# Performance work log

Measured on AMD Instinct MI355X. Metric: run time of the kernel, lower is better.

The kernel has to match this reference:

```python
import jax, jax.numpy as jnp
import numpy as np

B, C, H, W = 4, 256, 64, 64


def _radius_bias(h, w):
    # Attention_Radius: grid coords (x: 1..W, y: H..1), pairwise euclidean dist
    y = jnp.arange(h, 0, -1, dtype=jnp.float32)
    x = jnp.arange(1, w + 1, dtype=jnp.float32)
    yy, xx = jnp.meshgrid(y, x, indexing='ij')
    coords = jnp.stack([xx.reshape(-1), yy.reshape(-1)], axis=1)  # [N,2]
    diff = coords[:, None, :] - coords[None, :, :]                # [N,N,2]
    dist = jnp.sqrt(jnp.sum(diff * diff, axis=-1))                # [N,N]
    # Weight_Mapping: linearly map to [0.5,2] with inversion (far -> small)
    lo, hi = jnp.float32(0.5), jnp.float32(2.0)
    return hi - (dist - dist.min()) * (hi - lo) / (dist.max() - dist.min())


def setup_inputs() -> dict:
    key = jax.random.key(0)
    k1, k2, k3, k4 = jax.random.split(key, 4)
    scale = 1.0 / np.sqrt(C)
    return {
        'x': jax.random.normal(k1, (B, C, H, W), dtype=jnp.float32),
        'w_phi': jax.random.normal(k2, (C, C), dtype=jnp.float32) * scale,
        'w_theta': jax.random.normal(k3, (C, C), dtype=jnp.float32) * scale,
        'w_g': jax.random.normal(k4, (C, C), dtype=jnp.float32) * scale,
    }


def reference(x, w_phi, w_theta, w_g):
    b, c, h, w = x.shape
    n = h * w
    xf = x.reshape(b, c, n)                                  # [b,c,N]
    phi = jnp.einsum('dc,bcn->bdn', w_phi, xf)               # [b,c,N]
    theta = jnp.einsum('dc,bcn->bnd', w_theta, xf)           # [b,N,c]
    g = jnp.einsum('dc,bcn->bnd', w_g, xf)                   # [b,N,c]
    scores = jnp.einsum('bnc,bcm->bnm', theta, phi)          # [b,N,N]
    scores = _radius_bias(h, w) * scores                     # multiplicative radius bias
    attn = jax.nn.softmax(scores, axis=1)                    # NOTE: softmax over dim=1 (rows)
    out = jnp.einsum('bnm,bmc->bnc', attn, g)                # [b,N,c]
    out = out.transpose(0, 2, 1).reshape(b, c, h, w)
    return out + x
```

## Files before the change

kernel.cpp:

```cpp
#include <hip/hip_runtime.h>
#include <math.h>

typedef unsigned short ush;
typedef short short8 __attribute__((ext_vector_type(8)));
typedef int i32x4 __attribute__((ext_vector_type(4)));
typedef int i32x16 __attribute__((ext_vector_type(16)));
typedef float f32x16 __attribute__((ext_vector_type(16)));
typedef unsigned int u32;

namespace {
constexpr int B = 4, C = 256, N = 4096, NCH = 4;
constexpr size_t PL8 = (size_t)B * N * C;
constexpr size_t OFF_TH  = 0;
constexpr size_t OFF_TL  = PL8;
constexpr size_t OFF_PH  = 2 * PL8;
constexpr size_t OFF_PLO = 3 * PL8;
constexpr size_t OFF_G   = 4 * PL8;
constexpr size_t FOFF    = 4 * PL8 + (size_t)B * C * N * 2;
constexpr size_t F_PM = 0;
constexpr size_t F_PS = (size_t)B * NCH * N;
constexpr size_t F_M  = 2 * (size_t)B * NCH * N;

constexpr size_t OFF_XH = 26ull * 1024 * 1024;
constexpr size_t OFF_XL = OFF_XH + (size_t)B * N * C * 2;
constexpr size_t OFF_WH = OFF_XL + (size_t)B * N * C * 2;
constexpr size_t OFF_WL = OFF_WH + (size_t)3 * C * C * 2;
constexpr size_t WS_NEED = OFF_WL + (size_t)3 * C * C * 2;

constexpr float SCL = 8.0f / 127.0f;
constexpr float S2  = SCL * SCL;
constexpr float RB  = 1.5f / 89.09545f;
constexpr float L2E = 1.44269504f;
constexpr float BA2  = 2.0f * S2 * L2E;
constexpr float BBC2 = RB * S2 * L2E;
constexpr float C1  = 1.0f / 254.0f;
constexpr float INV_SCL = 127.0f / 8.0f;
}

#define MFMAI8(a, b, c)  __builtin_amdgcn_mfma_i32_32x32x32_i8((a), (b), (c), 0, 0, 0)
#define MFMABF(a, b, c)  __builtin_amdgcn_mfma_f32_32x32x16_bf16((a), (b), (c), 0, 0, 0)

#define WAITV(n) asm volatile("s_waitcnt vmcnt(" #n ")" ::: "memory")
#define WAITVL(n) asm volatile("s_waitcnt vmcnt(" #n ") lgkmcnt(0)" ::: "memory")
#define PBAR __builtin_amdgcn_s_barrier()

__device__ __forceinline__ float fast_exp2(float x) {
#if __has_builtin(__builtin_amdgcn_exp2f)
  return __builtin_amdgcn_exp2f(x);
#else
  float r; asm("v_exp_f32 %0, %1" : "=v"(r) : "v"(x)); return r;
#endif
}
__device__ __forceinline__ float fast_sqrt(float x) {
#if __has_builtin(__builtin_amdgcn_sqrtf)
  return __builtin_amdgcn_sqrtf(x);
#else
  float r; asm("v_sqrt_f32 %0, %1" : "=v"(r) : "v"(x)); return r;
#endif
}

__device__ __forceinline__ ush f2bf(float v) {
  u32 x = __float_as_uint(v);
  return (ush)((x + 0x7FFFu + ((x >> 16) & 1u)) >> 16);
}
__device__ __forceinline__ float bf2f(ush h) {
  return __uint_as_float(((u32)h) << 16);
}

__device__ __forceinline__ float score_i(int hh, int xx, int d2i) {
  float u = fmaf((float)xx, C1, (float)hh);
  float d = fast_sqrt((float)d2i);
  return fmaf(d, -BBC2, BA2) * u;
}

__device__ __forceinline__ void gload16(const void* g, void* l) {
  __builtin_amdgcn_global_load_lds(
      (const __attribute__((address_space(1))) u32*)(g),
      (__attribute__((address_space(3))) u32*)(l), 16, 0, 0);
}

__global__ __launch_bounds__(256) void proj_kernel(
    const float* __restrict__ x, const float* __restrict__ w_phi,
    const float* __restrict__ w_theta, const float* __restrict__ w_g,
    char* __restrict__ wsu8) {
  __shared__ float Wst[16][68];
  __shared__ float Xs[16][68];
  const int tid = threadIdx.x, tx = tid & 15, ty = tid >> 4;
  const int b = blockIdx.y / 3, p = blockIdx.y % 3;
  const int c0 = (blockIdx.x >> 6) * 64;
  const int nb = (blockIdx.x & 63) * 64;
  const float* w = (p == 0) ? w_theta : (p == 1) ? w_phi : w_g;

  float acc[4][4] = {};
  for (int kk = 0; kk < C; kk += 16) {
    {
      int r = tid >> 2, kq = (tid & 3) << 2;
      float4 v = *reinterpret_cast<const float4*>(&w[(size_t)(c0 + r) * C + kk + kq]);
      Wst[kq + 0][r] = v.x; Wst[kq + 1][r] = v.y;
      Wst[kq + 2][r] = v.z; Wst[kq + 3][r] = v.w;
    }
    {
      int k = tid >> 4, j4 = (tid & 15) << 2;
      *reinterpret_cast<float4*>(&Xs[k][j4]) =
          *reinterpret_cast<const float4*>(&x[((size_t)b * C + kk + k) * N + nb + j4]);
    }
    __syncthreads();
#pragma unroll
    for (int k2 = 0; k2 < 16; ++k2) {
      float4 av = *reinterpret_cast<const float4*>(&Wst[k2][ty << 2]);
      float4 bv = *reinterpret_cast<const float4*>(&Xs[k2][tx << 2]);
      float aa[4] = {av.x, av.y, av.z, av.w};
      float bb[4] = {bv.x, bv.y, bv.z, bv.w};
#pragma unroll
      for (int i = 0; i < 4; ++i)
#pragma unroll
        for (int j = 0; j < 4; ++j) acc[i][j] = fmaf(aa[i], bb[j], acc[i][j]);
    }
    __syncthreads();
  }

  if (p < 2) {
    char* hi = wsu8 + (p == 0 ? OFF_TH : OFF_PH) + (size_t)b * N * C;
    char* lo = wsu8 + (p == 0 ? OFF_TL : OFF_PLO) + (size_t)b * N * C;
#pragma unroll
    for (int j = 0; j < 4; ++j) {
      int n = nb + (tx << 2) + j;
      u32 ph = 0, pl = 0;
#pragma unroll
      for (int i = 0; i < 4; ++i) {
        float t = acc[i][j] * INV_SCL;
        int h = __float2int_rn(t);
        h = max(-127, min(127, h));
        int l = __float2int_rn((t - (float)h) * 254.0f);
        l = max(-127, min(127, l));
        ph |= ((u32)(h & 0xFF)) << (8 * i);
        pl |= ((u32)(l & 0xFF)) << (8 * i);
      }
      *(u32*)(hi + (size_t)n * C + c0 + (ty << 2)) = ph;
      *(u32*)(lo + (size_t)n * C + c0 + (ty << 2)) = pl;
    }
  } else {
    ush* gp = (ush*)(wsu8 + OFF_G) + (size_t)b * C * N;
#pragma unroll
    for (int i = 0; i < 4; ++i) {
      ushort4 pk;
      pk.x = f2bf(acc[i][0]); pk.y = f2bf(acc[i][1]);
      pk.z = f2bf(acc[i][2]); pk.w = f2bf(acc[i][3]);
      *reinterpret_cast<ushort4*>(&gp[(size_t)(c0 + (ty << 2) + i) * N + nb + (tx << 2)]) = pk;
    }
  }
}

__global__ __launch_bounds__(256) void split_x(
    const float* __restrict__ x, char* __restrict__ wsu8) {
  __shared__ float Ls[64 * 66];
  const int tid = threadIdx.x;
  const int n0 = blockIdx.x * 64, c0 = blockIdx.y * 64, b = blockIdx.z;
  const float* xb = x + ((size_t)b * C + c0) * N + n0;
#pragma unroll
  for (int i = 0; i < 4; ++i) {
    int fi = i * 256 + tid, cc = fi >> 4, c4 = fi & 15;
    float4 v = *reinterpret_cast<const float4*>(xb + (size_t)cc * N + c4 * 4);
    Ls[cc * 66 + c4 * 4 + 0] = v.x; Ls[cc * 66 + c4 * 4 + 1] = v.y;
    Ls[cc * 66 + c4 * 4 + 2] = v.z; Ls[cc * 66 + c4 * 4 + 3] = v.w;
  }
  __syncthreads();
  ush* XH = (ush*)(wsu8 + OFF_XH) + ((size_t)b * N + n0) * C + c0;
  ush* XL = (ush*)(wsu8 + OFF_XL) + ((size_t)b * N + n0) * C + c0;
#pragma unroll
  for (int i = 0; i < 4; ++i) {
    int oi = i * 256 + tid, n = oi >> 4, c4 = oi & 15;
    ushort4 hv, lv;
#pragma unroll
    for (int j = 0; j < 4; ++j) {
      float v = Ls[(c4 * 4 + j) * 66 + n];
      ush h = f2bf(v);
      ush l = f2bf(v - bf2f(h));
      (&hv.x)[j] = h; (&lv.x)[j] = l;
    }
    *reinterpret_cast<ushort4*>(XH + (size_t)n * C + c4 * 4) = hv;
    *reinterpret_cast<ushort4*>(XL + (size_t)n * C + c4 * 4) = lv;
  }
}

__global__ __launch_bounds__(256) void split_w(
    const float* __restrict__ w_phi, const float* __restrict__ w_theta,
    const float* __restrict__ w_g, char* __restrict__ wsu8) {
  int id = blockIdx.x * 256 + threadIdx.x;
  int p = id / 16384, e4 = id % 16384;
  const float* w = (p == 0) ? w_theta : (p == 1) ? w_phi : w_g;
  float4 v = *reinterpret_cast<const float4*>(w + (size_t)e4 * 4);
  ush* WH = (ush*)(wsu8 + OFF_WH) + (size_t)p * C * C + (size_t)e4 * 4;
  ush* WL = (ush*)(wsu8 + OFF_WL) + (size_t)p * C * C + (size_t)e4 * 4;
  ushort4 hv, lv;
  float vv[4] = {v.x, v.y, v.z, v.w};
#pragma unroll
  for (int j = 0; j < 4; ++j) {
    ush h = f2bf(vv[j]);
    ush l = f2bf(vv[j] - bf2f(h));
    (&hv.x)[j] = h; (&lv.x)[j] = l;
  }
  *reinterpret_cast<ushort4*>(WH) = hv;
  *reinterpret_cast<ushort4*>(WL) = lv;
}

__global__ __launch_bounds__(512) void proj_mfma(char* __restrict__ wsu8) {
  __shared__ __align__(16) char plds[131072];
  const int tid = threadIdx.x, lane = tid & 63, w = tid >> 6;
  const int l31 = lane & 31, lh5 = lane >> 5;
  const int wr = w >> 2, wc = w & 3;
  const int bx = blockIdx.x;
  const int db = (bx >> 5) * 64, nb = (bx & 31) * 128;
  const int b = blockIdx.y / 3, p = blockIdx.y % 3;
  const char* xh = wsu8 + OFF_XH + (size_t)b * N * C * 2;
  const char* xl = wsu8 + OFF_XL + (size_t)b * N * C * 2;
  const char* wh = wsu8 + OFF_WH + (size_t)p * C * C * 2;
  const char* wl = wsu8 + OFF_WL + (size_t)p * C * C * 2;
  char* const Wb = plds;
  char* const Xb = plds + 65536;

#pragma unroll
  for (int cix = 0; cix < 8; ++cix) {
    int pl = cix >> 2, ci = cix & 3;
    int glin = ci * 512 + tid;
    int d = glin >> 5, g = glin & 31;
    const char* src = (pl ? wl : wh) + (size_t)(db + d) * 512 + ((g ^ (d & 15)) << 4);
    gload16(src, Wb + pl * 32768 + ci * 8192 + (tid << 4));
  }
  auto stageX = [&](int ch, int buf) {
#pragma unroll
    for (int cix = 0; cix < 4; ++cix) {
      int pl = cix >> 1, ci = cix & 1;
      int glin = ci * 512 + tid;
      int n = glin >> 3, g = glin & 7;
      const char* src = (pl ? xl : xh) +
          (size_t)(nb + n) * 512 + ch * 128 + ((g ^ (n & 7)) << 4);
      gload16(src, Xb + buf * 32768 + pl * 16384 + ci * 8192 + (tid << 4));
    }
  };
  stageX(0, 0);
  __syncthreads();

  const int arow = wr * 32 + l31;
  const int brow = wc * 32 + l31;
  f32x16 acc = {};
  for (int ch = 0; ch < 4; ++ch) {
    if (ch < 3) stageX(ch + 1, (ch + 1) & 1);
    const char* XB = Xb + (ch & 1) * 32768;
    __builtin_amdgcn_s_setprio(1);
#pragma unroll
    for (int kt = 0; kt < 4; ++kt) {
      int slw = (ch * 4 + kt) * 2 + lh5;
      int oW = ((slw ^ (arow & 15)) << 4);
      short8 wa = *(const short8*)(Wb + arow * 512 + oW);
      short8 wb2 = *(const short8*)(Wb + 32768 + arow * 512 + oW);
      int slx = kt * 2 + lh5;
      int oX = ((slx ^ (brow & 7)) << 4);
      short8 xa = *(const short8*)(XB + brow * 128 + oX);
      short8 xb2 = *(const short8*)(XB + 16384 + brow * 128 + oX);
      acc = MFMABF(wa, xa, acc);
      acc = MFMABF(wa, xb2, acc);
      acc = MFMABF(wb2, xa, acc);
    }
    __builtin_amdgcn_s_setprio(0);
    __syncthreads();
  }

  const int n = nb + wc * 32 + l31;
  if (p < 2) {
    char* hi = wsu8 + (p == 0 ? OFF_TH : OFF_PH) + (size_t)b * N * C;
    char* lo = wsu8 + (p == 0 ? OFF_TL : OFF_PLO) + (size_t)b * N * C;
#pragma unroll
    for (int q = 0; q < 4; ++q) {
      u32 phv = 0, plv = 0;
#pragma unroll
      for (int j = 0; j < 4; ++j) {
        float t = acc[q * 4 + j] * INV_SCL;
        int h = __float2int_rn(t);
        h = max(-127, min(127, h));
        int l = __float2int_rn((t - (float)h) * 254.0f);
        l = max(-127, min(127, l));
        phv |= ((u32)(h & 0xFF)) << (8 * j);
        plv |= ((u32)(l & 0xFF)) << (8 * j);
      }
      int dd = db + wr * 32 + 8 * q + 4 * lh5;
      *(u32*)(hi + (size_t)n * C + dd) = phv;
      *(u32*)(lo + (size_t)n * C + dd) = plv;
    }
  } else {
    ush* gp = (ush*)(wsu8 + OFF_G) + (size_t)b * C * N;
#pragma unroll
    for (int r = 0; r < 16; ++r) {
      int dd = db + wr * 32 + (r & 3) + 8 * (r >> 2) + 4 * lh5;
      gp[(size_t)dd * N + n] = f2bf(acc[r]);
    }
  }
}

__global__ __launch_bounds__(512, 4) void stats_kernel(
    const char* __restrict__ wsu8, float* __restrict__ fws) {
  __shared__ __align__(16) char lds[65536];
  const int tid = threadIdx.x, lane = tid & 63, w = tid >> 6;
  const int l31 = lane & 31, lh5 = lane >> 5;
  const int wr = w >> 2, wc = w & 3;
  int flat = (blockIdx.z * NCH + blockIdx.y) * 32 + blockIdx.x;
  int nf = ((flat & 7) << 6) | (flat >> 3);
  const int b = nf >> 7, rem = nf & 127, chunk = rem >> 5, mt = rem & 31;
  const int mb = mt * 128, cbase = chunk * 1024;
  const size_t bo = (size_t)b * N * C;
  const char* th  = wsu8 + OFF_TH + bo;
  const char* tl  = wsu8 + OFF_TL + bo;
  const char* ph  = wsu8 + OFF_PH + bo;
  const char* plo = wsu8 + OFF_PLO + bo;

  const int brow = wc * 32 + l31;
  const int bswz = brow & 15;
  i32x4 FH[8];
  {
    const char* prh = ph + (size_t)(mb + brow) * C + lh5 * 16;
#pragma unroll
    for (int q = 0; q < 8; ++q) FH[q] = *(const i32x4*)(prh + q * 32);
  }
#pragma unroll
  for (int cix = 0; cix < 4; ++cix) {
    int rl = cix * 32 + w * 4 + (lane >> 4);
    int gc = lane & 15;
    const char* src = plo + (size_t)(mb + rl) * C + ((gc ^ (rl & 15)) << 4);
    gload16(src, lds + cix * 8192 + w * 1024 + lane * 16);
  }
  char* const T0 = lds + 32768;
  char* const T1 = lds + 49152;

  auto stage = [&](int s, char* dst) {
    int ntx = s >> 1, h = s & 1;
    int rl = w * 8 + (lane >> 3);
    int gc = lane & 7;
#pragma unroll
    for (int plane = 0; plane < 2; ++plane) {
      const char* src = (plane ? tl : th) +
          (size_t)(cbase + ntx * 64 + rl) * C + h * 128 + ((gc ^ (rl & 7)) << 4);
      gload16(src, dst + plane * 8192 + w * 1024 + lane * 16);
    }
  };
  stage(0, T0);
  __syncthreads();

  const int m = mb + brow;
  const int mcl = m & 63, mh = m >> 6;
  const int arow = wr * 32 + l31;
  const int aswz = arow & 7;
  const int nbl = wr * 32;
  float rmax = -3e38f, rsum = 0.0f;

  u32 dxp[8];
#pragma unroll
  for (int r2 = 0; r2 < 8; ++r2) {
    int r0i = 2 * r2, r1i = 2 * r2 + 1;
    int p0 = (r0i & 3) + 8 * (r0i >> 2) + 4 * lh5;
    int p1 = (r1i & 3) + 8 * (r1i >> 2) + 4 * lh5;
    int d0 = nbl + p0 - mcl, d1 = nbl + p1 - mcl;
    dxp[r2] = (u32)(d0 * d0) | ((u32)(d1 * d1) << 16);
  }

  char* Tc = T0; char* Tn = T1;
  for (int nt = 0; nt < 16; ++nt) {
    i32x16 HH = {}, XX = {};
#pragma unroll
    for (int h = 0; h < 2; ++h) {
      int p = nt * 2 + h;
      if (p < 31) stage(p + 1, Tn);
      __builtin_amdgcn_s_setprio(1);
#pragma unroll
      for (int kt = 0; kt < 4; ++kt) {
        int g = h * 4 + kt;
        int ga = (((kt * 2 + lh5) ^ aswz) << 4);
        i32x4 ah = *(const i32x4*)(Tc + arow * 128 + ga);
        i32x4 al = *(const i32x4*)(Tc + 8192 + arow * 128 + ga);
        int gb = (((g * 2 + lh5) ^ bswz) << 4);
        i32x4 bl = *(const i32x4*)(lds + brow * 256 + gb);
        HH = MFMAI8(ah, FH[g], HH);
        XX = MFMAI8(ah, bl, XX);
        XX = MFMAI8(al, FH[g], XX);
      }
      __builtin_amdgcn_s_setprio(0);
      if (h == 1) {
        int dyi = (cbase >> 6) + nt - mh;
        int dy2i = dyi * dyi;
        float bs[16];
#pragma unroll
        for (int r = 0; r < 16; ++r) {
          int d2i = (int)((dxp[r >> 1] >> ((r & 1) * 16)) & 0xFFFFu) + dy2i;
          bs[r] = score_i(HH[r], XX[r], d2i);
        }
        float m0 = fmaxf(fmaxf(fmaxf(bs[0], bs[1]), fmaxf(bs[2], bs[3])),
                         fmaxf(fmaxf(bs[4], bs[5]), fmaxf(bs[6], bs[7])));
        float m1 = fmaxf(fmaxf(fmaxf(bs[8], bs[9]), fmaxf(bs[10], bs[11])),
                         fmaxf(fmaxf(bs[12], bs[13]), fmaxf(bs[14], bs[15])));
        float nm = fmaxf(rmax, fmaxf(m0, m1));
#pragma unroll
        for (int r = 0; r < 16; ++r) bs[r] = fast_exp2(bs[r] - nm);
        float s0 = ((bs[0] + bs[1]) + (bs[2] + bs[3])) + ((bs[4] + bs[5]) + (bs[6] + bs[7]));
        float s1 = ((bs[8] + bs[9]) + (bs[10] + bs[11])) + ((bs[12] + bs[13]) + (bs[14] + bs[15]));
        rsum = fmaf(rsum, fast_exp2(rmax - nm), s0 + s1);
        rmax = nm;
      }
      __syncthreads();
      char* t = Tc; Tc = Tn; Tn = t;
    }
  }
  {
    float om = __shfl_xor(rmax, 32);
    float os = __shfl_xor(rsum, 32);
    float nm = fmaxf(rmax, om);
    rsum = rsum * fast_exp2(rmax - nm) + os * fast_exp2(om - nm);
    rmax = nm;
  }
  float* redM = (float*)lds;
  float* redS = (float*)(lds + 1024);
  if (lane < 32) {
    redM[wr * 128 + wc * 32 + l31] = rmax;
    redS[wr * 128 + wc * 32 + l31] = rsum;
  }
  __syncthreads();
  if (tid < 128) {
    float m0 = redM[tid], m1 = redM[128 + tid];
    float nm = fmaxf(m0, m1);
    float s = redS[tid] * fast_exp2(m0 - nm) + redS[128 + tid] * fast_exp2(m1 - nm);
    fws[F_PM + ((size_t)(b * NCH + chunk)) * N + mb + tid] = nm;
    fws[F_PS + ((size_t)(b * NCH + chunk)) * N + mb + tid] = s;
  }
}

__global__ __launch_bounds__(256) void finalize_stats(float* __restrict__ fws) {
  int id = blockIdx.x * 256 + threadIdx.x;
  if (id >= B * N) return;
  int b = id >> 12, m = id & (N - 1);
  float M = -3e38f;
#pragma unroll
  for (int ch = 0; ch < NCH; ++ch)
    M = fmaxf(M, fws[F_PM + (size_t)(b * NCH + ch) * N + m]);
  float S = 0.0f;
#pragma unroll
  for (int ch = 0; ch < NCH; ++ch)
    S += fws[F_PS + (size_t)(b * NCH + ch) * N + m] *
         fast_exp2(fws[F_PM + (size_t)(b * NCH + ch) * N + m] - M);
  fws[F_M + id] = M + __log2f(S);
}

__global__ __launch_bounds__(512, 1) void out_kernel(
    const float* __restrict__ x, float* __restrict__ out,
    const char* __restrict__ wsu8, const float* __restrict__ fws) {
  __shared__ __align__(16) char lds[131072];
  const int tid = threadIdx.x, lane = tid & 63, w = tid >> 6;
  const int l31 = lane & 31, lh5 = lane >> 5;
  const int wn = w >> 2, wm = w & 3;
  int flat = blockIdx.y * gridDim.x + blockIdx.x;
  int nf = ((flat & 7) << 5) | (flat >> 3);
  const int b = nf >> 6, ntile = nf & 63;
  const int n0 = ntile * 64;
  const size_t bo = (size_t)b * N * C;
  const char* th  = wsu8 + OFF_TH + bo;
  const char* tl  = wsu8 + OFF_TL + bo;
  const char* ph  = wsu8 + OFF_PH + bo;
  const char* plo = wsu8 + OFF_PLO + bo;
  const char* GPB = wsu8 + OFF_G + (size_t)b * C * N * 2;
  const float* Qv = fws + F_M + (size_t)b * N;

  char* const R0 = lds;
  char* const R1 = lds + 32768;
  char* const R2 = lds + 65536;
  char* const Pb = lds + 98304;
  char* const Qb = lds + 114688;

  const int arow = wn * 32 + l31;
  const int brow = wm * 32 + l31;
  const int grow = w * 32 + l31;
  const int bswz = brow & 7, gswz = grow & 7;
  const int mcl = (wm * 32 + l31) & 63;

  i32x4 TH[8], TL[8];
  {
    const char* trh = th + (size_t)(n0 + arow) * C + lh5 * 16;
    const char* trl = tl + (size_t)(n0 + arow) * C + lh5 * 16;
#pragma unroll
    for (int q = 0; q < 8; ++q) {
      TH[q] = *(const i32x4*)(trh + q * 32);
      TL[q] = *(const i32x4*)(trl + q * 32);
    }
  }
  u32 dxp[8];
#pragma unroll
  for (int r2 = 0; r2 < 8; ++r2) {
    int r0i = 2 * r2, r1i = 2 * r2 + 1;
    int p0i = wn * 32 + (r0i & 3) + 8 * (r0i >> 2) + 4 * lh5;
    int p1i = wn * 32 + (r1i & 3) + 8 * (r1i >> 2) + 4 * lh5;
    int d0 = p0i - mcl, d1 = p1i - mcl;
    dxp[r2] = (u32)(d0 * d0) | ((u32)(d1 * d1) << 16);
  }
#pragma unroll
  for (int i = 0; i < 2; ++i)
    gload16((const char*)Qv + i * 8192 + w * 1024 + lane * 16,
            Qb + i * 8192 + w * 1024 + lane * 16);

  auto stagePhi = [&](int mrow0, int khalf, char* dst) {
#pragma unroll
    for (int cix = 0; cix < 4; ++cix) {
      int plane = cix >> 1, q = cix & 1;
      int rl = q * 64 + w * 8 + (lane >> 3);
      int gc = lane & 7;
      const char* src = (plane ? plo : ph) +
          (size_t)(mrow0 + rl) * C + khalf * 128 + ((gc ^ (rl & 7)) << 4);
      gload16(src, dst + plane * 16384 + q * 8192 + w * 1024 + lane * 16);
    }
  };
  auto stageG = [&](int m0g, char* dst) {
#pragma unroll
    for (int cix = 0; cix < 4; ++cix) {
      int rl = cix * 64 + w * 8 + (lane >> 3);
      int gc = lane & 7;
      const char* src = GPB + (size_t)rl * (N * 2) + (size_t)m0g * 2 + ((gc ^ (rl & 7)) << 4);
      gload16(src, dst + cix * 8192 + w * 1024 + lane * 16);
    }
  };

  stagePhi(0, 0, R0);
  stagePhi(0, 1, R1);
  WAITV(4);
  PBAR;

  f32x16 oacc0 = {}, oacc1 = {};
  char* Bc = R0; char* Bn = R1; char* Bn2 = R2;

  for (int mc = 0; mc < 32; ++mc) {
    const int m0 = mc * 128;
    i32x16 HH = {}, XX = {};
    const int mg = m0 + wm * 32 + l31;
    const float Qm = *(const float*)(Qb + 4 * mg);

    stageG(m0, Bn2);
    __builtin_amdgcn_s_setprio(1);
#pragma unroll
    for (int kt = 0; kt < 4; ++kt) {
      int gb = (((kt * 2 + lh5) ^ bswz) << 4);
      i32x4 bh = *(const i32x4*)(Bc + brow * 128 + gb);
      i32x4 bl = *(const i32x4*)(Bc + 16384 + brow * 128 + gb);
      HH = MFMAI8(TH[kt], bh, HH);
      XX = MFMAI8(TH[kt], bl, XX);
      XX = MFMAI8(TL[kt], bh, XX);
    }
    __builtin_amdgcn_s_setprio(0);
    WAITV(4); PBAR;

    stageG(m0 + 64, Bc);
    __builtin_amdgcn_s_setprio(1);
#pragma unroll
    for (int kt = 0; kt < 4; ++kt) {
      int gb = (((kt * 2 + lh5) ^ bswz) << 4);
      i32x4 bh = *(const i32x4*)(Bn + brow * 128 + gb);
      i32x4 bl = *(const i32x4*)(Bn + 16384 + brow * 128 + gb);
      HH = MFMAI8(TH[4 + kt], bh, HH);
      XX = MFMAI8(TH[4 + kt], bl, XX);
      XX = MFMAI8(TL[4 + kt], bh, XX);
    }
    __builtin_amdgcn_s_setprio(0);
    {
      const int pcol = wm * 32 + l31;
      const int gP = pcol >> 3, bP = (pcol & 7) << 1;
      int dyi = ntile - (mg >> 6);
      int dy2i = dyi * dyi;
#pragma unroll
      for (int r = 0; r < 16; ++r) {
        int prow = wn * 32 + (r & 3) + 8 * (r >> 2) + 4 * lh5;
        int d2i = (int)((dxp[r >> 1] >> ((r & 1) * 16)) & 0xFFFFu) + dy2i;
        float bs = score_i(HH[r], XX[r], d2i);
        float pv = fast_exp2(bs - Qm);
        *(ush*)(Pb + prow * 256 + (((gP ^ (prow & 15)) << 4)) + bP) = f2bf(pv);
      }
    }
    WAITVL(4); PBAR;

    if (mc < 31) stagePhi(m0 + 128, 0, Bn);
    __builtin_amdgcn_s_setprio(1);
#pragma unroll
    for (int t2 = 0; t2 < 4; ++t2) {
      int gG = (((t2 * 2 + lh5) ^ gswz) << 4);
      short8 gb = *(const short8*)(Bn2 + grow * 128 + gG);
      {
        int gP0 = ((((t2 * 2 + lh5) ^ (l31 & 15)) << 4));
        short8 pa = *(const short8*)(Pb + l31 * 256 + gP0);
        oacc0 = MFMABF(pa, gb, oacc0);
      }
      {
        int ar = 32 + l31;
        int gP1 = ((((t2 * 2 + lh5) ^ (ar & 15)) << 4));
        short8 pa = *(const short8*)(Pb + ar * 256 + gP1);
        oacc1 = MFMABF(pa, gb, oacc1);
      }
    }
    __builtin_amdgcn_s_setprio(0);
    if (mc < 31) { WAITV(4); } else { WAITV(0); }
    PBAR;

    if (mc < 31) stagePhi(m0 + 128, 1, Bn2);
    __builtin_amdgcn_s_setprio(1);
#pragma unroll
    for (int t2 = 0; t2 < 4; ++t2) {
      int gG = (((t2 * 2 + lh5) ^ gswz) << 4);
      short8 gb = *(const short8*)(Bc + grow * 128 + gG);
      {
        int gP0 = ((((8 + t2 * 2 + lh5) ^ (l31 & 15)) << 4));
        short8 pa = *(const short8*)(Pb + l31 * 256 + gP0);
        oacc0 = MFMABF(pa, gb, oacc0);
      }
      {
        int ar = 32 + l31;
        int gP1 = ((((8 + t2 * 2 + lh5) ^ (ar & 15)) << 4));
        short8 pa = *(const short8*)(Pb + ar * 256 + gP1);
        oacc1 = MFMABF(pa, gb, oacc1);
      }
    }
    __builtin_amdgcn_s_setprio(0);
    if (mc < 31) { WAITV(4); } else { WAITV(0); }
    PBAR;

    char* t = Bc; Bc = Bn; Bn = Bn2; Bn2 = t;
  }

  float* Tr = (float*)lds;
  const int c = w * 32 + l31;
#pragma unroll
  for (int r = 0; r < 16; ++r) {
    int crow = (r & 3) + 8 * (r >> 2) + 4 * lh5;
    Tr[c * 65 + crow] = oacc0[r];
    Tr[c * 65 + 32 + crow] = oacc1[r];
  }
  __syncthreads();
  const float* xb = x + (size_t)b * C * N;
  float* ob = out + (size_t)b * C * N;
  for (int e = tid; e < 16384; e += 512) {
    int cc = e >> 6, nl = e & 63;
    size_t idx = (size_t)cc * N + n0 + nl;
    ob[idx] = Tr[cc * 65 + nl] + xb[idx];
  }
}

extern "C" void kernel_launch(void* const* d_in, const int* in_sizes, int n_in,
                              void* d_out, int out_size, void* d_ws, size_t ws_size,
                              hipStream_t stream) {
  const float* x       = (const float*)d_in[0];
  const float* w_phi   = (const float*)d_in[1];
  const float* w_theta = (const float*)d_in[2];
  const float* w_g     = (const float*)d_in[3];
  float* out = (float*)d_out;
  char* wsu8 = (char*)d_ws;
  float* fws = (float*)(wsu8 + FOFF);

  if (ws_size >= WS_NEED) {
    split_x<<<dim3(64, 4, 4), 256, 0, stream>>>(x, wsu8);
    split_w<<<dim3(192), 256, 0, stream>>>(w_phi, w_theta, w_g, wsu8);
    proj_mfma<<<dim3(128, 12), 512, 0, stream>>>(wsu8);
  } else {
    proj_kernel<<<dim3(256, 12), 256, 0, stream>>>(x, w_phi, w_theta, w_g, wsu8);
  }
  stats_kernel<<<dim3(32, NCH, B), 512, 0, stream>>>(wsu8, fws);
  finalize_stats<<<dim3(B * N / 256), 256, 0, stream>>>(fws);
  out_kernel<<<dim3(64, B), 512, 0, stream>>>(x, out, wsu8, fws);
}
```

Baseline: 211.6 us.

## Load phi tiles straight into registers and shrink LDS for two blocks per CU

The out_kernel no longer stages phi high/low tiles through LDS. Each lane now loads its phi fragments directly from global memory into registers, prefetched one chunk ahead. This frees 32 KB of LDS, so the G tile uses a two-buffer scheme and launch bounds ask for two blocks per CU. The aim is more occupancy and less LDS traffic and barrier work, at the cost of higher register pressure (16 extra i32x4 registers) and uncoalesced per-lane global loads of phi. The wait counts and barriers are also reworked, which carries a risk of race conditions on the reused G buffers.

```diff
diff --git a/kernel.cpp b/kernel.cpp
--- a/kernel.cpp
+++ b/kernel.cpp
@@ -447,10 +447,10 @@
   fws[F_M + id] = M + __log2f(S);
 }
 
-__global__ __launch_bounds__(512, 1) void out_kernel(
+__global__ __launch_bounds__(512, 2) void out_kernel(
     const float* __restrict__ x, float* __restrict__ out,
     const char* __restrict__ wsu8, const float* __restrict__ fws) {
-  __shared__ __align__(16) char lds[131072];
+  __shared__ __align__(16) char lds[98304];
   const int tid = threadIdx.x, lane = tid & 63, w = tid >> 6;
   const int l31 = lane & 31, lh5 = lane >> 5;
   const int wn = w >> 2, wm = w & 3;
@@ -466,16 +466,15 @@
   const char* GPB = wsu8 + OFF_G + (size_t)b * C * N * 2;
   const float* Qv = fws + F_M + (size_t)b * N;
 
-  char* const R0 = lds;
-  char* const R1 = lds + 32768;
-  char* const R2 = lds + 65536;
-  char* const Pb = lds + 98304;
-  char* const Qb = lds + 114688;
+  char* const Ga = lds;
+  char* const Gb = lds + 32768;
+  char* const Pb = lds + 65536;
+  char* const Qb = lds + 81920;
 
   const int arow = wn * 32 + l31;
   const int brow = wm * 32 + l31;
   const int grow = w * 32 + l31;
-  const int bswz = brow & 7, gswz = grow & 7;
+  const int gswz = grow & 7;
   const int mcl = (wm * 32 + l31) & 63;
 
   i32x4 TH[8], TL[8];
@@ -502,15 +501,14 @@
     gload16((const char*)Qv + i * 8192 + w * 1024 + lane * 16,
             Qb + i * 8192 + w * 1024 + lane * 16);
 
-  auto stagePhi = [&](int mrow0, int khalf, char* dst) {
-#pragma unroll
-    for (int cix = 0; cix < 4; ++cix) {
-      int plane = cix >> 1, q = cix & 1;
-      int rl = q * 64 + w * 8 + (lane >> 3);
-      int gc = lane & 7;
-      const char* src = (plane ? plo : ph) +
-          (size_t)(mrow0 + rl) * C + khalf * 128 + ((gc ^ (rl & 7)) << 4);
-      gload16(src, dst + plane * 16384 + q * 8192 + w * 1024 + lane * 16);
+  i32x4 Bh[8], Bl[8];
+  const char* phw = ph  + (size_t)brow * C + lh5 * 16;
+  const char* plw = plo + (size_t)brow * C + lh5 * 16;
+  auto ldphi = [&](int m0i) {
+#pragma unroll
+    for (int q = 0; q < 8; ++q) {
+      Bh[q] = *(const i32x4*)(phw + (size_t)m0i * C + q * 32);
+      Bl[q] = *(const i32x4*)(plw + (size_t)m0i * C + q * 32);
     }
   };
   auto stageG = [&](int m0g, char* dst) {
@@ -523,44 +521,34 @@
     }
   };
 
-  stagePhi(0, 0, R0);
-  stagePhi(0, 1, R1);
-  WAITV(4);
+  ldphi(0);
+  WAITV(0);
   PBAR;
 
   f32x16 oacc0 = {}, oacc1 = {};
-  char* Bc = R0; char* Bn = R1; char* Bn2 = R2;
 
   for (int mc = 0; mc < 32; ++mc) {
     const int m0 = mc * 128;
-    i32x16 HH = {}, XX = {};
     const int mg = m0 + wm * 32 + l31;
     const float Qm = *(const float*)(Qb + 4 * mg);
-
-    stageG(m0, Bn2);
+    i32x16 HH = {}, XX = {};
+
+    stageG(m0, Ga);
     __builtin_amdgcn_s_setprio(1);
 #pragma unroll
     for (int kt = 0; kt < 4; ++kt) {
-      int gb = (((kt * 2 + lh5) ^ bswz) << 4);
-      i32x4 bh = *(const i32x4*)(Bc + brow * 128 + gb);
-      i32x4 bl = *(const i32x4*)(Bc + 16384 + brow * 128 + gb);
-      HH = MFMAI8(TH[kt], bh, HH);
-      XX = MFMAI8(TH[kt], bl, XX);
-      XX = MFMAI8(TL[kt], bh, XX);
+      HH = MFMAI8(TH[kt], Bh[kt], HH);
+      XX = MFMAI8(TH[kt], Bl[kt], XX);
+      XX = MFMAI8(TL[kt], Bh[kt], XX);
     }
     __builtin_amdgcn_s_setprio(0);
-    WAITV(4); PBAR;
-
-    stageG(m0 + 64, Bc);
+    stageG(m0 + 64, Gb);
     __builtin_amdgcn_s_setprio(1);
 #pragma unroll
-    for (int kt = 0; kt < 4; ++kt) {
-      int gb = (((kt * 2 + lh5) ^ bswz) << 4);
-      i32x4 bh = *(const i32x4*)(Bn + brow * 128 + gb);
-      i32x4 bl = *(const i32x4*)(Bn + 16384 + brow * 128 + gb);
-      HH = MFMAI8(TH[4 + kt], bh, HH);
-      XX = MFMAI8(TH[4 + kt], bl, XX);
-      XX = MFMAI8(TL[4 + kt], bh, XX);
+    for (int kt = 4; kt < 8; ++kt) {
+      HH = MFMAI8(TH[kt], Bh[kt], HH);
+      XX = MFMAI8(TH[kt], Bl[kt], XX);
+      XX = MFMAI8(TL[kt], Bh[kt], XX);
     }
     __builtin_amdgcn_s_setprio(0);
     {
@@ -579,12 +567,12 @@
     }
     WAITVL(4); PBAR;
 
-    if (mc < 31) stagePhi(m0 + 128, 0, Bn);
+    if (mc < 31) ldphi(m0 + 128);
     __builtin_amdgcn_s_setprio(1);
 #pragma unroll
     for (int t2 = 0; t2 < 4; ++t2) {
       int gG = (((t2 * 2 + lh5) ^ gswz) << 4);
-      short8 gb = *(const short8*)(Bn2 + grow * 128 + gG);
+      short8 gb = *(const short8*)(Ga + grow * 128 + gG);
       {
         int gP0 = ((((t2 * 2 + lh5) ^ (l31 & 15)) << 4));
         short8 pa = *(const short8*)(Pb + l31 * 256 + gP0);
@@ -598,15 +586,14 @@
       }
     }
     __builtin_amdgcn_s_setprio(0);
-    if (mc < 31) { WAITV(4); } else { WAITV(0); }
+    if (mc < 31) { WAITV(16); } else { WAITV(0); }
     PBAR;
 
-    if (mc < 31) stagePhi(m0 + 128, 1, Bn2);
     __builtin_amdgcn_s_setprio(1);
 #pragma unroll
     for (int t2 = 0; t2 < 4; ++t2) {
       int gG = (((t2 * 2 + lh5) ^ gswz) << 4);
-      short8 gb = *(const short8*)(Bc + grow * 128 + gG);
+      short8 gb = *(const short8*)(Gb + grow * 128 + gG);
       {
         int gP0 = ((((8 + t2 * 2 + lh5) ^ (l31 & 15)) << 4));
         short8 pa = *(const short8*)(Pb + l31 * 256 + gP0);
@@ -620,10 +607,7 @@
       }
     }
     __builtin_amdgcn_s_setprio(0);
-    if (mc < 31) { WAITV(4); } else { WAITV(0); }
     PBAR;
-
-    char* t = Bc; Bc = Bn; Bn = Bn2; Bn2 = t;
   }
 
   float* Tr = (float*)lds;
```

Result: slower. 296.5 us (+40.1%).
